# Optimization experiments

Measured on AMD Instinct MI355X. Metric: run time of the kernel, lower is better.

## Reference

```python
import jax, jax.numpy as jnp
import numpy as np

B, C, H, W = 16, 1024, 32, 32


def setup_inputs() -> dict:
    key = jax.random.key(0)
    ka, kb, kc = jax.random.split(key, 3)
    a = jax.random.normal(ka, (B, C, H, W), dtype=jnp.float32)
    b = jax.random.normal(kb, (B, C, H, W), dtype=jnp.float32)
    c = jax.random.normal(kc, (B, C, H, W), dtype=jnp.float32)
    return {"a": a, "b": b, "c": c}


def reference(a, b, c):
    Bn, Cn = a.shape[0], a.shape[1]
    a_f = a.reshape(Bn, Cn, -1)  # [B, C, HW]
    b_f = b.reshape(Bn, Cn, -1)
    c_f = c.reshape(Bn, Cn, -1)
    # channel-attention scores: [B, C, C]
    scores = jnp.einsum('bik,bjk->bij', b_f, c_f)
    mid = jax.nn.softmax(scores, axis=-1)
    out = jnp.einsum('bij,bjk->bik', mid, a_f)  # [B, C, HW]
    out = out.reshape(a.shape) + a  # residual add
    return out
```

## Files before the change

### kernel.cpp

```cpp
#include <hip/hip_runtime.h>
#include <hip/hip_bf16.h>
#include <stdint.h>

#define BATCH 16
#define CDIM 1024
#define HWDIM 1024
#define PSTRIDE 2048
#define TILE_E (256 * 64)
#define NTK 16

typedef _Float16 half_t;
typedef _Float16 half8 __attribute__((ext_vector_type(8)));
typedef float floatx4 __attribute__((ext_vector_type(4)));

__device__ static inline void gld_lds16(const half_t* g, half_t* l) {
    __builtin_amdgcn_global_load_lds(
        (__attribute__((address_space(1))) void*)(void*)g,
        (__attribute__((address_space(3))) void*)l, 16, 0, 0);
}

__device__ __forceinline__ half8 ld8(const char* p) { return *(const half8*)p; }

template <int MB, int NB>
__device__ __forceinline__ void mfma16(floatx4 (&acc)[8][4],
                                       const half8 (&a4)[4][2],
                                       const half8 (&b2)[2][2]) {
#pragma unroll
    for (int mt = 0; mt < 4; ++mt)
#pragma unroll
        for (int nt = 0; nt < 2; ++nt)
#pragma unroll
            for (int ks = 0; ks < 2; ++ks)
                acc[MB + mt][NB + nt] = __builtin_amdgcn_mfma_f32_16x16x32_f16(
                    a4[mt][ks], b2[nt][ks], acc[MB + mt][NB + nt], 0, 0, 0);
}

__device__ __forceinline__ void gemm8p(const half_t* __restrict__ Ag, size_t sA,
                                       const half_t* __restrict__ Bg, size_t sB,
                                       int i0, int j0,
                                       half_t* lA, half_t* lB,
                                       floatx4 (&acc)[8][4]) {
    const int tid = threadIdx.x;
    const int lane = tid & 63;
    const int wave = tid >> 6;
    const int wm = wave >> 2, wn = wave & 3;
    const int fr = lane & 15, hi = lane >> 4;
    const int sw = (fr & 7) << 4;
    const int o0 = fr * 128 + ((hi * 16) ^ sw);
    const int o1 = fr * 128 + ((hi * 16 + 64) ^ sw);

    const int r0 = tid >> 3;
    const int scol = ((tid & 7) ^ (r0 & 7)) * 8;
    const half_t* pa = Ag + (size_t)(i0 + r0) * sA + scol;
    const half_t* pb = Bg + (size_t)(j0 + r0) * sB + scol;

#pragma unroll
    for (int a = 0; a < 8; ++a)
#pragma unroll
        for (int b = 0; b < 4; ++b) acc[a][b] = (floatx4){0.f, 0.f, 0.f, 0.f};

#define STG_A(tt, h)                                                      \
    do {                                                                  \
        const half_t* g_ = pa + (size_t)(h) * 128 * sA + (tt) * 64;       \
        half_t* l_ = lA + ((tt) & 1) * TILE_E + (h) * 8192 + tid * 8;     \
        gld_lds16(g_, l_);                                                \
        gld_lds16(g_ + 64 * sA, l_ + 4096);                               \
    } while (0)
#define STG_B(tt, h)                                                      \
    do {                                                                  \
        const half_t* g_ = pb + (size_t)(h) * 128 * sB + (tt) * 64;       \
        half_t* l_ = lB + ((tt) & 1) * TILE_E + (h) * 8192 + tid * 8;     \
        gld_lds16(g_, l_);                                                \
        gld_lds16(g_ + 64 * sB, l_ + 4096);                               \
    } while (0)

    STG_A(0, 0); STG_B(0, 0); STG_A(0, 1); STG_B(0, 1);
    STG_B(1, 0); STG_A(1, 0); STG_B(1, 1);
    asm volatile("s_waitcnt vmcnt(6)" ::: "memory");
    __builtin_amdgcn_s_barrier();

    half8 af[4][2], bf0[2][2], bf1[2][2];

#pragma unroll 2
    for (int t = 0; t < NTK; ++t) {
        const char* aw = (const char*)(lA + (t & 1) * TILE_E) + wm * 8192;
        const char* bw = (const char*)(lB + (t & 1) * TILE_E) + wn * 4096;

#pragma unroll
        for (int mt = 0; mt < 4; ++mt) {
            af[mt][0] = ld8(aw + mt * 2048 + o0);
            af[mt][1] = ld8(aw + mt * 2048 + o1);
        }
#pragma unroll
        for (int nt = 0; nt < 2; ++nt) {
            bf0[nt][0] = ld8(bw + nt * 2048 + o0);
            bf0[nt][1] = ld8(bw + nt * 2048 + o1);
        }
        if (t + 1 < NTK) STG_A(t + 1, 1);
        __builtin_amdgcn_s_barrier();
        asm volatile("s_waitcnt lgkmcnt(0)" ::: "memory");
        __builtin_amdgcn_s_setprio(1);
        mfma16<0, 0>(acc, af, bf0);
        __builtin_amdgcn_s_setprio(0);
        __builtin_amdgcn_sched_barrier(0);
        __builtin_amdgcn_s_barrier();

#pragma unroll
        for (int nt = 0; nt < 2; ++nt) {
            bf1[nt][0] = ld8(bw + 16384 + nt * 2048 + o0);
            bf1[nt][1] = ld8(bw + 16384 + nt * 2048 + o1);
        }
        if (t + 2 < NTK) STG_B(t + 2, 0);
        __builtin_amdgcn_s_barrier();
        asm volatile("s_waitcnt lgkmcnt(0)" ::: "memory");
        __builtin_amdgcn_s_setprio(1);
        mfma16<0, 2>(acc, af, bf1);
        __builtin_amdgcn_s_setprio(0);
        __builtin_amdgcn_sched_barrier(0);
        __builtin_amdgcn_s_barrier();

#pragma unroll
        for (int mt = 0; mt < 4; ++mt) {
            af[mt][0] = ld8(aw + 16384 + mt * 2048 + o0);
            af[mt][1] = ld8(aw + 16384 + mt * 2048 + o1);
        }
        if (t + 2 < NTK) STG_A(t + 2, 0);
        __builtin_amdgcn_s_barrier();
        asm volatile("s_waitcnt lgkmcnt(0)" ::: "memory");
        __builtin_amdgcn_s_setprio(1);
        mfma16<4, 2>(acc, af, bf1);
        __builtin_amdgcn_s_setprio(0);
        __builtin_amdgcn_sched_barrier(0);
        __builtin_amdgcn_s_barrier();

        if (t + 2 < NTK) STG_B(t + 2, 1);
        if (t < NTK - 2)
            asm volatile("s_waitcnt vmcnt(6)" ::: "memory");
        else
            asm volatile("s_waitcnt vmcnt(0)" ::: "memory");
        __builtin_amdgcn_s_barrier();
        __builtin_amdgcn_s_setprio(1);
        mfma16<4, 0>(acc, af, bf0);
        __builtin_amdgcn_s_setprio(0);
        __builtin_amdgcn_sched_barrier(0);
        __builtin_amdgcn_s_barrier();
    }
#undef STG_A
#undef STG_B
}

__device__ __forceinline__ void tile_coords(int& bz, int& i0, int& j0) {
    const int flat = blockIdx.x + (blockIdx.y << 4);
    const int w = ((flat & 7) << 5) + (flat >> 3);
    bz = w >> 4;
    const int tl = w & 15;
    i0 = (tl & 3) << 8;
    j0 = (tl >> 2) << 8;
}

__global__ __launch_bounds__(256) void k_prep(const float* __restrict__ Bm,
                                              const float* __restrict__ Cm,
                                              half_t* __restrict__ dst) {
    const size_t N = (size_t)BATCH * CDIM * HWDIM;
    const size_t NV = N / 4;
    const float* src = blockIdx.y ? Cm : Bm;
    half_t* d = dst + (size_t)blockIdx.y * N;
    const size_t stride = (size_t)gridDim.x * 256;
    for (size_t i = (size_t)blockIdx.x * 256 + threadIdx.x; i < NV; i += stride) {
        float4 f = ((const float4*)src)[i];
        half_t h[4];
        h[0] = (half_t)f.x; h[1] = (half_t)f.y;
        h[2] = (half_t)f.z; h[3] = (half_t)f.w;
        ((uint2*)d)[i] = *(const uint2*)h;
    }
}

__global__ __launch_bounds__(256) void k_softmax(float* __restrict__ S) {
    const int wave = threadIdx.x >> 6;
    const int lane = threadIdx.x & 63;
    float* rp = S + ((size_t)blockIdx.x * 4 + wave) * CDIM;

    float4 v[4];
#pragma unroll
    for (int j = 0; j < 4; ++j) v[j] = ((const float4*)rp)[lane + 64 * j];

    float m = -1e30f;
#pragma unroll
    for (int j = 0; j < 4; ++j)
        m = fmaxf(m, fmaxf(fmaxf(v[j].x, v[j].y), fmaxf(v[j].z, v[j].w)));
#pragma unroll
    for (int off = 32; off > 0; off >>= 1) m = fmaxf(m, __shfl_xor(m, off));

    float e[4][4];
    float s = 0.f;
#pragma unroll
    for (int j = 0; j < 4; ++j) {
        e[j][0] = __expf(v[j].x - m); e[j][1] = __expf(v[j].y - m);
        e[j][2] = __expf(v[j].z - m); e[j][3] = __expf(v[j].w - m);
        s += e[j][0] + e[j][1] + e[j][2] + e[j][3];
    }
#pragma unroll
    for (int off = 32; off > 0; off >>= 1) s += __shfl_xor(s, off);
    const float inv = 1.0f / s;

#pragma unroll
    for (int j = 0; j < 4; ++j) {
        half_t p[4];
        p[0] = (half_t)(e[j][0] * inv); p[1] = (half_t)(e[j][1] * inv);
        p[2] = (half_t)(e[j][2] * inv); p[3] = (half_t)(e[j][3] * inv);
        ((uint2*)rp)[lane + 64 * j] = *(const uint2*)p;
    }
}

__global__ __launch_bounds__(256) void k_transpose(const float* __restrict__ A,
                                                   half_t* __restrict__ SP) {
    const int bz = blockIdx.z;
    const int t0 = blockIdx.x * 64;
    const int j0 = blockIdx.y * 64;
    const float* Ap = A + (size_t)bz * CDIM * HWDIM;
    half_t* Atp = SP + (size_t)bz * CDIM * PSTRIDE + 1024;

    __shared__ half_t tile[64][68];
    const int lr = threadIdx.x >> 4;
    const int lc = (threadIdx.x & 15) * 4;
#pragma unroll
    for (int r = 0; r < 4; ++r) {
        const float* src = Ap + (size_t)(j0 + lr + r * 16) * HWDIM + t0 + lc;
        float4 f = *(const float4*)src;
        half_t t4[4];
        t4[0] = (half_t)f.x; t4[1] = (half_t)f.y;
        t4[2] = (half_t)f.z; t4[3] = (half_t)f.w;
        *(uint2*)&tile[lr + r * 16][lc] = *(const uint2*)t4;
    }
    __syncthreads();
#pragma unroll
    for (int r = 0; r < 4; ++r) {
        const int trow = lr + r * 16;
        half_t tmp[4];
#pragma unroll
        for (int e = 0; e < 4; ++e) tmp[e] = tile[lc + e][trow];
        *(uint2*)(Atp + (size_t)(t0 + trow) * PSTRIDE + j0 + lc) = *(uint2*)tmp;
    }
}

__global__ __launch_bounds__(512, 2) void k_gemm1(const half_t* __restrict__ Bh,
                                                  const half_t* __restrict__ Ch,
                                                  float* __restrict__ S) {
    __shared__ half_t lA[2 * TILE_E];
    __shared__ half_t lB[2 * TILE_E];
    int bz, i0, j0;
    tile_coords(bz, i0, j0);

    floatx4 acc[8][4];
    gemm8p(Bh + (size_t)bz * CDIM * HWDIM, HWDIM,
           Ch + (size_t)bz * CDIM * HWDIM, HWDIM, i0, j0, lA, lB, acc);

    float* Sp = S + (size_t)bz * CDIM * CDIM;
    const int lane = threadIdx.x & 63;
    const int wave = threadIdx.x >> 6;
    const int wm = wave >> 2, wn = wave & 3;
    const int er = (lane >> 4) * 4;
    const int ec = lane & 15;
#pragma unroll
    for (int mt = 0; mt < 8; ++mt) {
        const int row0 = i0 + ((mt >> 2) << 7) + wm * 64 + (mt & 3) * 16 + er;
#pragma unroll
        for (int nt = 0; nt < 4; ++nt) {
            const int col = j0 + ((nt >> 1) << 7) + wn * 32 + (nt & 1) * 16 + ec;
            float* dst = Sp + (size_t)row0 * CDIM + col;
#pragma unroll
            for (int r = 0; r < 4; ++r) dst[(size_t)r * CDIM] = acc[mt][nt][r];
        }
    }
}

__global__ __launch_bounds__(512, 2) void k_gemm2(const half_t* __restrict__ SP,
                                                  const float* __restrict__ Aorig,
                                                  float* __restrict__ Out) {
    __shared__ half_t lA[2 * TILE_E];
    __shared__ half_t lB[2 * TILE_E];
    int bz, i0, t0;
    tile_coords(bz, i0, t0);

    const half_t* Pp = SP + (size_t)bz * CDIM * PSTRIDE;
    const half_t* Bp = Pp + 1024;

    floatx4 acc[8][4];
    gemm8p(Pp, PSTRIDE, Bp, PSTRIDE, i0, t0, lA, lB, acc);

    const float* ap = Aorig + (size_t)bz * CDIM * HWDIM;
    float* op = Out + (size_t)bz * CDIM * HWDIM;
    const int lane = threadIdx.x & 63;
    const int wave = threadIdx.x >> 6;
    const int wm = wave >> 2, wn = wave & 3;
    const int er = (lane >> 4) * 4;
    const int ec = lane & 15;
#pragma unroll
    for (int mt = 0; mt < 8; ++mt) {
        const int row0 = i0 + ((mt >> 2) << 7) + wm * 64 + (mt & 3) * 16 + er;
#pragma unroll
        for (int nt = 0; nt < 4; ++nt) {
            const int col = t0 + ((nt >> 1) << 7) + wn * 32 + (nt & 1) * 16 + ec;
#pragma unroll
            for (int r = 0; r < 4; ++r) {
                const size_t idx = (size_t)(row0 + r) * HWDIM + col;
                op[idx] = acc[mt][nt][r] + ap[idx];
            }
        }
    }
}

extern "C" void kernel_launch(void* const* d_in, const int* in_sizes, int n_in,
                              void* d_out, int out_size, void* d_ws, size_t ws_size,
                              hipStream_t stream) {
    const float* a = (const float*)d_in[0];
    const float* b = (const float*)d_in[1];
    const float* c = (const float*)d_in[2];
    float* out = (float*)d_out;

    float* S = (float*)d_ws;
    half_t* bc16 = (half_t*)d_out;

    k_prep<<<dim3(2048, 2), 256, 0, stream>>>(b, c, bc16);
    k_gemm1<<<dim3(16, 16), 512, 0, stream>>>(
        bc16, bc16 + (size_t)BATCH * CDIM * HWDIM, S);
    k_softmax<<<dim3(BATCH * CDIM / 4), 256, 0, stream>>>(S);
    k_transpose<<<dim3(16, 16, 16), 256, 0, stream>>>(a, (half_t*)S);
    k_gemm2<<<dim3(16, 16), 512, 0, stream>>>((const half_t*)S, a, out);
}
```

Before: 310.8 us.

## Fuse fp32-to-fp16 conversion of b and c into the first GEMM's load pipeline

Removes the separate k_prep kernel that converted b and c to fp16 in global memory. The first GEMM now loads fp32 tiles straight into registers, converts them to fp16 and writes them to LDS inside a rewritten software pipeline with register staging. This saves a full read-and-write pass over two 64 MiB inputs and one kernel launch. In exchange the GEMM reads twice as many bytes per tile, each tile is re-read by several blocks, and staging through registers adds register pressure and VALU work inside the main loop.

```diff
diff --git a/kernel.cpp b/kernel.cpp
--- a/kernel.cpp
+++ b/kernel.cpp
@@ -33,6 +33,25 @@
             for (int ks = 0; ks < 2; ++ks)
                 acc[MB + mt][NB + nt] = __builtin_amdgcn_mfma_f32_16x16x32_f16(
                     a4[mt][ks], b2[nt][ks], acc[MB + mt][NB + nt], 0, 0, 0);
+}
+
+struct St4 { float4 a, b, c, d; };
+
+__device__ __forceinline__ void stld(const float* g, size_t s, St4& r) {
+    r.a = *(const float4*)g;
+    r.b = *(const float4*)(g + 4);
+    r.c = *(const float4*)(g + 64 * s);
+    r.d = *(const float4*)(g + 64 * s + 4);
+}
+
+__device__ __forceinline__ void stwr(half_t* l, const St4& r) {
+    half8 v0, v1;
+    v0[0] = (half_t)r.a.x; v0[1] = (half_t)r.a.y; v0[2] = (half_t)r.a.z; v0[3] = (half_t)r.a.w;
+    v0[4] = (half_t)r.b.x; v0[5] = (half_t)r.b.y; v0[6] = (half_t)r.b.z; v0[7] = (half_t)r.b.w;
+    v1[0] = (half_t)r.c.x; v1[1] = (half_t)r.c.y; v1[2] = (half_t)r.c.z; v1[3] = (half_t)r.c.w;
+    v1[4] = (half_t)r.d.x; v1[5] = (half_t)r.d.y; v1[6] = (half_t)r.d.z; v1[7] = (half_t)r.d.w;
+    *(half8*)l = v0;
+    *(half8*)(l + 4096) = v1;
 }
 
 __device__ __forceinline__ void gemm8p(const half_t* __restrict__ Ag, size_t sA,
@@ -149,6 +168,120 @@
 #undef STG_B
 }
 
+__device__ __forceinline__ void gemm8p32(const float* __restrict__ Ag, size_t sA,
+                                         const float* __restrict__ Bg, size_t sB,
+                                         int i0, int j0,
+                                         half_t* lA, half_t* lB,
+                                         floatx4 (&acc)[8][4]) {
+    const int tid = threadIdx.x;
+    const int lane = tid & 63;
+    const int wave = tid >> 6;
+    const int wm = wave >> 2, wn = wave & 3;
+    const int fr = lane & 15, hi = lane >> 4;
+    const int sw = (fr & 7) << 4;
+    const int o0 = fr * 128 + ((hi * 16) ^ sw);
+    const int o1 = fr * 128 + ((hi * 16 + 64) ^ sw);
+
+    const int r0 = tid >> 3;
+    const int scol = ((tid & 7) ^ (r0 & 7)) * 8;
+    const float* pa = Ag + (size_t)(i0 + r0) * sA + scol;
+    const float* pb = Bg + (size_t)(j0 + r0) * sB + scol;
+
+#pragma unroll
+    for (int a = 0; a < 8; ++a)
+#pragma unroll
+        for (int b = 0; b < 4; ++b) acc[a][b] = (floatx4){0.f, 0.f, 0.f, 0.f};
+
+    St4 sA1, sB0, sA0, sB1;
+
+    stld(pa, sA, sA0);                     stwr(lA + tid * 8, sA0);
+    stld(pb, sB, sB0);                     stwr(lB + tid * 8, sB0);
+    stld(pa + (size_t)128 * sA, sA, sA1);  stwr(lA + 8192 + tid * 8, sA1);
+    stld(pb + (size_t)128 * sB, sB, sB1);  stwr(lB + 8192 + tid * 8, sB1);
+    stld(pb + 64, sB, sB0);                stwr(lB + TILE_E + tid * 8, sB0);
+    stld(pa + 64, sA, sA0);                stwr(lA + TILE_E + tid * 8, sA0);
+    stld(pb + (size_t)128 * sB + 64, sB, sB1);
+    asm volatile("s_waitcnt lgkmcnt(0)" ::: "memory");
+    __builtin_amdgcn_s_barrier();
+
+    half8 af[4][2], bf0[2][2], bf1[2][2];
+
+#pragma unroll 2
+    for (int t = 0; t < NTK; ++t) {
+        const char* aw = (const char*)(lA + (t & 1) * TILE_E) + wm * 8192;
+        const char* bw = (const char*)(lB + (t & 1) * TILE_E) + wn * 4096;
+        half_t* nA = lA + ((t + 1) & 1) * TILE_E + tid * 8;
+        half_t* nB = lB + ((t + 1) & 1) * TILE_E + tid * 8;
+        half_t* cA = lA + (t & 1) * TILE_E + tid * 8;
+        half_t* cB = lB + (t & 1) * TILE_E + tid * 8;
+
+#pragma unroll
+        for (int mt = 0; mt < 4; ++mt) {
+            af[mt][0] = ld8(aw + mt * 2048 + o0);
+            af[mt][1] = ld8(aw + mt * 2048 + o1);
+        }
+#pragma unroll
+        for (int nt = 0; nt < 2; ++nt) {
+            bf0[nt][0] = ld8(bw + nt * 2048 + o0);
+            bf0[nt][1] = ld8(bw + nt * 2048 + o1);
+        }
+        if (t + 1 < NTK) {
+            stwr(nB + 8192, sB1);
+            stld(pa + (size_t)128 * sA + (t + 1) * 64, sA, sA1);
+        }
+        __builtin_amdgcn_s_barrier();
+        asm volatile("s_waitcnt lgkmcnt(0)" ::: "memory");
+        __builtin_amdgcn_s_setprio(1);
+        mfma16<0, 0>(acc, af, bf0);
+        __builtin_amdgcn_s_setprio(0);
+        __builtin_amdgcn_sched_barrier(0);
+        __builtin_amdgcn_s_barrier();
+
+#pragma unroll
+        for (int nt = 0; nt < 2; ++nt) {
+            bf1[nt][0] = ld8(bw + 16384 + nt * 2048 + o0);
+            bf1[nt][1] = ld8(bw + 16384 + nt * 2048 + o1);
+        }
+        if (t + 1 < NTK) stwr(nA + 8192, sA1);
+        if (t + 2 < NTK) stld(pb + (t + 2) * 64, sB, sB0);
+        __builtin_amdgcn_s_barrier();
+        asm volatile("s_waitcnt lgkmcnt(0)" ::: "memory");
+        __builtin_amdgcn_s_setprio(1);
+        mfma16<0, 2>(acc, af, bf1);
+        __builtin_amdgcn_s_setprio(0);
+        __builtin_amdgcn_sched_barrier(0);
+        __builtin_amdgcn_s_barrier();
+
+#pragma unroll
+        for (int mt = 0; mt < 4; ++mt) {
+            af[mt][0] = ld8(aw + 16384 + mt * 2048 + o0);
+            af[mt][1] = ld8(aw + 16384 + mt * 2048 + o1);
+        }
+        if (t + 2 < NTK) {
+            stwr(cB, sB0);
+            stld(pa + (t + 2) * 64, sA, sA0);
+        }
+        __builtin_amdgcn_s_barrier();
+        asm volatile("s_waitcnt lgkmcnt(0)" ::: "memory");
+        __builtin_amdgcn_s_setprio(1);
+        mfma16<4, 2>(acc, af, bf1);
+        __builtin_amdgcn_s_setprio(0);
+        __builtin_amdgcn_sched_barrier(0);
+        __builtin_amdgcn_s_barrier();
+
+        if (t + 2 < NTK) {
+            stwr(cA, sA0);
+            stld(pb + (size_t)128 * sB + (t + 2) * 64, sB, sB1);
+        }
+        __builtin_amdgcn_s_barrier();
+        __builtin_amdgcn_s_setprio(1);
+        mfma16<4, 0>(acc, af, bf0);
+        __builtin_amdgcn_s_setprio(0);
+        __builtin_amdgcn_sched_barrier(0);
+        __builtin_amdgcn_s_barrier();
+    }
+}
+
 __device__ __forceinline__ void tile_coords(int& bz, int& i0, int& j0) {
     const int flat = blockIdx.x + (blockIdx.y << 4);
     const int w = ((flat & 7) << 5) + (flat >> 3);
@@ -158,23 +291,6 @@
     j0 = (tl >> 2) << 8;
 }
 
-__global__ __launch_bounds__(256) void k_prep(const float* __restrict__ Bm,
-                                              const float* __restrict__ Cm,
-                                              half_t* __restrict__ dst) {
-    const size_t N = (size_t)BATCH * CDIM * HWDIM;
-    const size_t NV = N / 4;
-    const float* src = blockIdx.y ? Cm : Bm;
-    half_t* d = dst + (size_t)blockIdx.y * N;
-    const size_t stride = (size_t)gridDim.x * 256;
-    for (size_t i = (size_t)blockIdx.x * 256 + threadIdx.x; i < NV; i += stride) {
-        float4 f = ((const float4*)src)[i];
-        half_t h[4];
-        h[0] = (half_t)f.x; h[1] = (half_t)f.y;
-        h[2] = (half_t)f.z; h[3] = (half_t)f.w;
-        ((uint2*)d)[i] = *(const uint2*)h;
-    }
-}
-
 __global__ __launch_bounds__(256) void k_softmax(float* __restrict__ S) {
     const int wave = threadIdx.x >> 6;
     const int lane = threadIdx.x & 63;
@@ -243,8 +359,8 @@
     }
 }
 
-__global__ __launch_bounds__(512, 2) void k_gemm1(const half_t* __restrict__ Bh,
-                                                  const half_t* __restrict__ Ch,
+__global__ __launch_bounds__(512, 2) void k_gemm1(const float* __restrict__ Bm,
+                                                  const float* __restrict__ Cm,
                                                   float* __restrict__ S) {
     __shared__ half_t lA[2 * TILE_E];
     __shared__ half_t lB[2 * TILE_E];
@@ -252,8 +368,8 @@
     tile_coords(bz, i0, j0);
 
     floatx4 acc[8][4];
-    gemm8p(Bh + (size_t)bz * CDIM * HWDIM, HWDIM,
-           Ch + (size_t)bz * CDIM * HWDIM, HWDIM, i0, j0, lA, lB, acc);
+    gemm8p32(Bm + (size_t)bz * CDIM * HWDIM, HWDIM,
+             Cm + (size_t)bz * CDIM * HWDIM, HWDIM, i0, j0, lA, lB, acc);
 
     float* Sp = S + (size_t)bz * CDIM * CDIM;
     const int lane = threadIdx.x & 63;
@@ -319,11 +435,8 @@
     float* out = (float*)d_out;
 
     float* S = (float*)d_ws;
-    half_t* bc16 = (half_t*)d_out;
-
-    k_prep<<<dim3(2048, 2), 256, 0, stream>>>(b, c, bc16);
-    k_gemm1<<<dim3(16, 16), 512, 0, stream>>>(
-        bc16, bc16 + (size_t)BATCH * CDIM * HWDIM, S);
+
+    k_gemm1<<<dim3(16, 16), 512, 0, stream>>>(b, c, S);
     k_softmax<<<dim3(BATCH * CDIM / 4), 256, 0, stream>>>(S);
     k_transpose<<<dim3(16, 16, 16), 256, 0, stream>>>(a, (half_t*)S);
     k_gemm2<<<dim3(16, 16), 512, 0, stream>>>((const half_t*)S, a, out);
```

After: 366.8 us. +18.0%, slower.
